# Kernel tuning notes

Hardware: AMD Instinct MI355X
Metric: run time of the kernel (lower is better)

## Reference

```python
import jax, jax.numpy as jnp
from jax import lax
import numpy as np


def setup_inputs() -> dict:
    key = jax.random.key(0)
    ks = iter(jax.random.split(key, 48))

    def w(shape):
        fan = shape[0] if len(shape) == 2 else int(np.prod(shape[1:]))
        return jax.random.normal(next(ks), shape, jnp.float32) / np.sqrt(fan)

    def b(n):
        return jax.random.normal(next(ks), (n,), jnp.float32) * 0.01

    T = 16
    return dict(
        search=jax.random.normal(next(ks), (3, 383, 287), jnp.float32),
        exemplars=jax.random.normal(next(ks), (T, 3, 383, 287), jnp.float32),
        # AlexNet features (random-weight stand-in for pretrained)
        aw1=w((64, 3, 11, 11)), ab1=b(64),
        aw2=w((192, 64, 5, 5)), ab2=b(192),
        aw3=w((384, 192, 3, 3)), ab3=b(384),
        aw4=w((256, 384, 3, 3)), ab4=b(256),
        aw5=w((256, 256, 3, 3)), ab5=b(256),
        # conv_deconv: Conv1d(256,256,3,p=1) -> MaxPool1d(88) -> ConvTranspose1d(256,256,88)
        wcd=w((256, 256, 3)), bcd=b(256),
        wt=w((256, 256, 88)), bt=b(256),
        # st_gcn: GCN(256, 512, 256)
        ws1=w((256, 512)), bs1=b(512),
        ws2=w((512, 256)), bs2=b(256),
        # g, h: 1x1 Conv1d(256,256) == linear maps
        wg=w((256, 256)), bg=b(256),
        wh=w((256, 256)), bh=b(256),
        # ct_gcn: GCN(256, 384, 256)
        wc1=w((256, 384)), bc1=b(384),
        wc2=w((384, 256)), bc2=b(256),
    )


def _gct_forward(search, exemplars, aw1, ab1, aw2, ab2, aw3, ab3, aw4, ab4,
                 aw5, ab5, wcd, bcd, wt, bt, ws1, bs1, ws2, bs2,
                 wg, bg, wh, bh, wc1, bc1, wc2, bc2):
    f32 = jnp.float32

    def conv2d(x, w, bias, s, p):
        y = lax.conv_general_dilated(x, w, (s, s), [(p, p), (p, p)],
                                     dimension_numbers=('NCHW', 'OIHW', 'NCHW'))
        return y + bias[None, :, None, None]

    def maxpool(x):  # k=3, s=2, VALID (AlexNet pools)
        return lax.reduce_window(x, -jnp.inf, lax.max, (1, 1, 3, 3), (1, 1, 2, 2), 'VALID')

    def features(x):
        x = maxpool(jax.nn.relu(conv2d(x, aw1, ab1, 4, 2)))
        x = maxpool(jax.nn.relu(conv2d(x, aw2, ab2, 1, 2)))
        x = jax.nn.relu(conv2d(x, aw3, ab3, 1, 1))
        x = jax.nn.relu(conv2d(x, aw4, ab4, 1, 1))
        x = maxpool(jax.nn.relu(conv2d(x, aw5, ab5, 1, 1)))
        return x

    lrelu = lambda v: jax.nn.leaky_relu(v, 0.01)

    X = features(search[None])          # [1,256,11,8]
    Z = features(exemplars)             # [T,256,11,8]
    T = Z.shape[0]
    D = X.shape[1]                      # 256
    M = X.shape[2] * X.shape[3]         # 88
    Xf = X.reshape(D, M)                # [256,88]
    Zf = Z.reshape(T, D, M)             # [T,256,88]

    # conv_deconv branch: conv1d(k=3,p=1) -> global maxpool -> conv_transpose(k=M)
    xc = lax.conv_general_dilated(Xf[None], wcd, (1,), [(1, 1)],
                                  dimension_numbers=('NCH', 'OIH', 'NCH'))[0] + bcd[:, None]
    v = jnp.max(xc, axis=1)                              # [256]
    X_hat = jnp.einsum('i,iok->ok', v, wt) + bt[:, None]  # [256,88]

    # spatiotemporal graph: A[i+T*j, i+T*k]=1 for j!=k; self-loops for t!=0
    TM = T * M
    n = jnp.arange(TM)
    same_t = (n[:, None] % T) == (n[None, :] % T)
    diff_s = (n[:, None] // T) != (n[None, :] // T)
    A1 = (same_t & diff_s).astype(f32) + jnp.diag((n % T != 0).astype(f32))

    # st GCN over TM nodes (node n = t + T*m -> spatial-major flatten)
    nodes = Zf.transpose(2, 0, 1).reshape(TM, D)          # [TM,256]
    h1 = lrelu(A1 @ (nodes @ ws1) + bs1)                  # [TM,512]
    h2 = lrelu(A1 @ (h1 @ ws2) + bs2)                     # [TM,256]
    V1 = jnp.max(h2.reshape(M, T, D), axis=1).T           # temporal max-pool -> [256,88]

    # dynamic cross-track graph: pairwise g/h affinities + row softmax (fused)
    Vx = V1 + X_hat                                       # [256,88]
    G = wg @ Vx + bg[:, None]                             # [256,88]
    Hh = wh @ Vx + bh[:, None]                            # [256,88]
    A2 = jax.nn.softmax(Hh.T @ G, axis=1)                 # [88,88], A2[j,i]=g(i).h(j)

    # ct GCN
    xv = V1.T                                             # [88,256]
    c1 = lrelu(A2 @ (xv @ wc1) + bc1)                     # [88,384]
    V2 = lrelu(A2 @ (c1 @ wc2) + bc2).T                   # [256,88]

    # F.conv2d(X[1,256,11,8], V2[1,256,11,8]) -> full-overlap correlation = scalar
    R = jnp.sum(Xf * V2).reshape(1, 1, 1, 1)
    return R


def reference(search, exemplars, aw1, ab1, aw2, ab2, aw3, ab3, aw4, ab4,
              aw5, ab5, wcd, bcd, wt, bt, ws1, bs1, ws2, bs2,
              wg, bg, wh, bh, wc1, bc1, wc2, bc2):
    return _gct_forward(search, exemplars, aw1, ab1, aw2, ab2, aw3, ab3, aw4, ab4,
                        aw5, ab5, wcd, bcd, wt, bt, ws1, bs1, ws2, bs2,
                        wg, bg, wh, bh, wc1, bc1, wc2, bc2)
```

## Files before the change

kernel.cpp:

```cpp
#include <hip/hip_runtime.h>
#include <hip/hip_bf16.h>
#include <math.h>

#define BATCH 17
#define T_EX 16
#define H0 383
#define W0 287
#define C1 64
#define H1 95
#define W1 71
#define H1P 47
#define W1P 35
#define C2 192
#define H2P 23
#define W2P 17
#define C3 384
#define C45 256
#define H5P 11
#define W5P 8
#define DD 256
#define MM 88
#define TM 1408

#define HP1 389
#define WP1 292

typedef unsigned short ushort_t;
typedef __attribute__((ext_vector_type(8))) short short8;
typedef __attribute__((ext_vector_type(4))) float f32x4;

__device__ __forceinline__ float lrelu(float v) { return v > 0.f ? v : 0.01f * v; }

__device__ __forceinline__ ushort_t f2bf(float f) {
    unsigned int u = __float_as_uint(f);
    unsigned int r = (u + 0x7fffu + ((u >> 16) & 1u)) >> 16;
    return (ushort_t)r;
}
__device__ __forceinline__ float b2f(ushort_t b) {
    return __uint_as_float(((unsigned int)b) << 16);
}
__device__ __forceinline__ short8 ld16(const ushort_t* p) { return *(const short8*)p; }
__device__ __forceinline__ short8 ld2x8(const ushort_t* p) {
    union { uint2 u[2]; short8 s; } uu;
    uu.u[0] = *(const uint2*)p;
    uu.u[1] = *(const uint2*)(p + 4);
    return uu.s;
}
__device__ __forceinline__ void async_cp16(ushort_t* l, const ushort_t* g) {
    __builtin_amdgcn_global_load_lds(
        (const __attribute__((address_space(1))) void*)g,
        (__attribute__((address_space(3))) void*)l, 16, 0, 0);
}

__device__ __forceinline__ void wprep_dev(const float* __restrict__ w,
                                          ushort_t* __restrict__ out,
                                          int KH, int KWl, int KWr, int CINl, int CINr,
                                          int NKS, int OCr, int idx) {
    int c = idx & 255;
    int rest = idx >> 8;
    int ks = rest % NKS;
    int ocb = rest / NKS;
    int k8 = c >> 6, m = c & 63;
    int oc = ocb * 64 + m;
    int KWC = KWl * CINl;
    ushort_t* o = out + (size_t)idx * 8;
#pragma unroll
    for (int j = 0; j < 8; ++j) {
        int kg = ks * 32 + k8 * 8 + j;
        int ky = kg / KWC; int rem = kg - ky * KWC;
        int kx = rem / CINl; int ic = rem - kx * CINl;
        float v = 0.f;
        if (oc < OCr && ky < KH && kx < KWr && ic < CINr)
            v = w[(((size_t)oc * CINr + ic) * KH + ky) * KWr + kx];
        o[j] = f2bf(v);
    }
}

__global__ void prep1_wp1_k(const float* __restrict__ search, const float* __restrict__ exemp,
                            ushort_t* __restrict__ out, const float* __restrict__ w1,
                            ushort_t* __restrict__ WT) {
    const int pb = (BATCH * HP1 * WP1 + 255) / 256;
    if ((int)blockIdx.x >= pb) {
        int idx = (blockIdx.x - pb) * 256 + threadIdx.x;
        if (idx < 4608) wprep_dev(w1, WT, 11, 12, 11, 4, 3, 18, 64, idx);
        return;
    }
    int idx = blockIdx.x * 256 + threadIdx.x;
    if (idx >= BATCH * HP1 * WP1) return;
    int x = idx % WP1; int t = idx / WP1;
    int y = t % HP1; int b = t / HP1;
    ushort4 o = {0, 0, 0, 0};
    int ix = x - 2, iy = y - 2;
    if (ix >= 0 && ix < W0 && iy >= 0 && iy < H0) {
        const float* src = (b == 0) ? search : exemp + (size_t)(b - 1) * 3 * H0 * W0;
        const int hw = H0 * W0;
        o.x = f2bf(src[iy * W0 + ix]);
        o.y = f2bf(src[hw + iy * W0 + ix]);
        o.z = f2bf(src[2 * hw + iy * W0 + ix]);
    }
    *(ushort4*)&out[(size_t)idx * 4] = o;
}

__global__ void wprep_k(const float* __restrict__ w, ushort_t* __restrict__ out,
                        int KH, int KWl, int KWr, int CINl, int CINr,
                        int NKS, int nch, int OCr,
                        float4* __restrict__ zp, int zn4) {
    const int wb = (nch + 255) >> 8;
    if ((int)blockIdx.x >= wb) {
        int z = (blockIdx.x - wb) * 256 + threadIdx.x;
        if (z < zn4) zp[z] = (float4){0.f, 0.f, 0.f, 0.f};
        return;
    }
    int idx = blockIdx.x * 256 + threadIdx.x;
    if (idx >= nch) return;
    wprep_dev(w, out, KH, KWl, KWr, CINl, CINr, NKS, OCr, idx);
}

__global__ void pool_wp_k(const ushort_t* __restrict__ in, ushort_t* __restrict__ out,
                          int C, int Hin, int Win, int Hout, int Wout,
                          int OHp, int OWp, int OPAD,
                          float4* __restrict__ zp, int zn4,
                          const float* __restrict__ w, ushort_t* __restrict__ WT,
                          int KH, int KWl, int KWr, int CINl, int CINr,
                          int NKS, int nch, int OCr) {
    const int total = BATCH * C * OHp * OWp;
    const int pb = (total + 255) >> 8;
    const int zb = (zn4 + 255) >> 8;
    int bx = blockIdx.x;
    if (bx >= pb + zb) {
        int idx = (bx - pb - zb) * 256 + threadIdx.x;
        if (idx < nch) wprep_dev(w, WT, KH, KWl, KWr, CINl, CINr, NKS, OCr, idx);
        return;
    }
    if (bx >= pb) {
        int z = (bx - pb) * 256 + threadIdx.x;
        if (z < zn4) zp[z] = (float4){0.f, 0.f, 0.f, 0.f};
        return;
    }
    int idx = bx * 256 + threadIdx.x;
    if (idx >= total) return;
    int c = idx % C; int r = idx / C;
    int x = r % OWp; r /= OWp;
    int y = r % OHp; int b = r / OHp;
    int iy = y - OPAD, ix = x - OPAD;
    ushort_t v = 0;
    if (iy >= 0 && iy < Hout && ix >= 0 && ix < Wout) {
        const int rs = Win * C;
        const ushort_t* p = in + (((size_t)b * Hin + 2 * iy) * Win + 2 * ix) * C + c;
        float m = b2f(p[0]);
        m = fmaxf(m, b2f(p[C])); m = fmaxf(m, b2f(p[2 * C]));
        m = fmaxf(m, b2f(p[rs])); m = fmaxf(m, b2f(p[rs + C])); m = fmaxf(m, b2f(p[rs + 2 * C]));
        m = fmaxf(m, b2f(p[2 * rs])); m = fmaxf(m, b2f(p[2 * rs + C])); m = fmaxf(m, b2f(p[2 * rs + 2 * C]));
        v = f2bf(m);
    }
    out[idx] = v;
}

template <int STRIDE, bool A16>
__global__ __launch_bounds__(256) void conv_mfma14(
    const ushort_t* __restrict__ inp, const ushort_t* __restrict__ wt,
    const float* __restrict__ bias, ushort_t* __restrict__ out,
    int Hp, int Wp, int C, int Wout, int HW, int Ntot, int NKS2, int KWl,
    int OHp, int OWp, int OPAD, int COUT) {
    const int tid = threadIdx.x;
    const int wv = tid >> 6, lane = tid & 63;
    const int quad = lane >> 4, l16 = lane & 15;
    const int wr = wv >> 1, wc = wv & 1;
    const int n_blk = blockIdx.x * 64;
    const int ocb = blockIdx.y;

    __shared__ ushort_t As[2][4096];
    __shared__ ushort_t Bs[2][4096];
    __shared__ int offs[432];

    const int KWC = KWl * C;
    for (int g = tid; g < NKS2 * 8; g += 256) {
        int kg = g * 8;
        int ky = kg / KWC; int rem = kg - ky * KWC;
        int kx = rem / C; int c8 = rem - kx * C;
        offs[g] = (ky * Wp + kx) * C + c8;
    }

    const size_t HWC = (size_t)Hp * Wp * C;
    const int g8 = lane & 7, po = lane >> 3;
    const ushort_t* bsrc0 = nullptr; const ushort_t* bsrc1 = nullptr;
    const ushort_t* lsrc = nullptr;
    int ws0 = 0, ws1 = 0;
    if constexpr (A16) {
        int np0 = n_blk + wv * 16 + po;      if (np0 >= Ntot) np0 = Ntot - 1;
        int np1 = n_blk + wv * 16 + 8 + po;  if (np1 >= Ntot) np1 = Ntot - 1;
        int b0 = np0 / HW, p0 = np0 - b0 * HW;
        int b1 = np1 / HW, p1 = np1 - b1 * HW;
        int oy0 = p0 / Wout, ox0 = p0 - oy0 * Wout;
        int oy1 = p1 / Wout, ox1 = p1 - oy1 * Wout;
        bsrc0 = inp + (size_t)b0 * HWC + (size_t)(oy0 * STRIDE * Wp + ox0 * STRIDE) * C;
        bsrc1 = inp + (size_t)b1 * HWC + (size_t)(oy1 * STRIDE * Wp + ox1 * STRIDE) * C;
        ws0 = g8 * 512 + (((wv * 16 + po) ^ g8) * 8);
        ws1 = g8 * 512 + (((wv * 16 + 8 + po) ^ g8) * 8);
    } else {
        int n0 = n_blk + lane; if (n0 >= Ntot) n0 = Ntot - 1;
        int b0 = n0 / HW, p0 = n0 - b0 * HW;
        int oy = p0 / Wout, ox = p0 - oy * Wout;
        lsrc = inp + (size_t)b0 * HWC + (size_t)(oy * STRIDE * Wp + ox * STRIDE) * C;
    }

    f32x4 acc[2][2];
#pragma unroll
    for (int am = 0; am < 2; ++am)
#pragma unroll
        for (int bn = 0; bn < 2; ++bn) acc[am][bn] = (f32x4){0.f, 0.f, 0.f, 0.f};

    const ushort_t* wblk = wt + (size_t)ocb * (size_t)NKS2 * 4096;

    __syncthreads();

    {
        const ushort_t* aS = wblk + tid * 8;
        async_cp16(&As[0][tid * 8], aS);
        async_cp16(&As[0][2048 + tid * 8], aS + 2048);
        if constexpr (A16) {
            *(short8*)&Bs[0][ws0] = ld16(bsrc0 + offs[g8]);
            *(short8*)&Bs[0][ws1] = ld16(bsrc1 + offs[g8]);
        } else {
            const int o0 = offs[wv], o1 = offs[4 + wv];
            *(short8*)&Bs[0][tid * 8] = ld2x8(lsrc + o0);
            *(short8*)&Bs[0][2048 + tid * 8] = ld2x8(lsrc + o1);
        }
    }
    __syncthreads();

    for (int ks2 = 0; ks2 < NKS2; ++ks2) {
        const int cur = ks2 & 1, nxt = cur ^ 1;
        const bool more = (ks2 + 1 < NKS2);
        short8 rb0, rb1;
        if (more) {
            const ushort_t* aS = wblk + (size_t)(ks2 + 1) * 4096 + tid * 8;
            async_cp16(&As[nxt][tid * 8], aS);
            async_cp16(&As[nxt][2048 + tid * 8], aS + 2048);
            if constexpr (A16) {
                rb0 = ld16(bsrc0 + offs[(ks2 + 1) * 8 + g8]);
                rb1 = ld16(bsrc1 + offs[(ks2 + 1) * 8 + g8]);
            } else {
                const int o0 = offs[(ks2 + 1) * 8 + wv], o1 = offs[(ks2 + 1) * 8 + 4 + wv];
                *(short8*)&Bs[nxt][tid * 8] = ld2x8(lsrc + o0);
                *(short8*)&Bs[nxt][2048 + tid * 8] = ld2x8(lsrc + o1);
            }
        }
#pragma unroll
        for (int h = 0; h < 2; ++h) {
            const short8 a0 = *(const short8*)&As[cur][h * 2048 + (quad * 64 + wr * 32 + l16) * 8];
            const short8 a1 = *(const short8*)&As[cur][h * 2048 + (quad * 64 + wr * 32 + 16 + l16) * 8];
            short8 b0, b1;
            if constexpr (A16) {
                b0 = *(const short8*)&Bs[cur][h * 2048 + quad * 512 + (((wc * 32 + l16) ^ (h * 4 + quad)) * 8)];
                b1 = *(const short8*)&Bs[cur][h * 2048 + quad * 512 + (((wc * 32 + 16 + l16) ^ (h * 4 + quad)) * 8)];
            } else {
                b0 = *(const short8*)&Bs[cur][h * 2048 + (quad * 64 + wc * 32 + l16) * 8];
                b1 = *(const short8*)&Bs[cur][h * 2048 + (quad * 64 + wc * 32 + 16 + l16) * 8];
            }
            acc[0][0] = __builtin_amdgcn_mfma_f32_16x16x32_bf16(a0, b0, acc[0][0], 0, 0, 0);
            acc[0][1] = __builtin_amdgcn_mfma_f32_16x16x32_bf16(a0, b1, acc[0][1], 0, 0, 0);
            acc[1][0] = __builtin_amdgcn_mfma_f32_16x16x32_bf16(a1, b0, acc[1][0], 0, 0, 0);
            acc[1][1] = __builtin_amdgcn_mfma_f32_16x16x32_bf16(a1, b1, acc[1][1], 0, 0, 0);
        }
        if constexpr (A16) {
            if (more) {
                *(short8*)&Bs[nxt][ws0] = rb0;
                *(short8*)&Bs[nxt][ws1] = rb1;
            }
        }
        __syncthreads();
    }

    const int oc0 = ocb * 64 + wr * 32 + quad * 4;
#pragma unroll
    for (int bn = 0; bn < 2; ++bn) {
        int n = n_blk + wc * 32 + bn * 16 + l16;
        if (n < Ntot) {
            int bb = n / HW; int pix = n - bb * HW;
            int y = pix / Wout, x = pix - y * Wout;
            size_t base = (((size_t)bb * OHp + y + OPAD) * OWp + x + OPAD) * COUT;
#pragma unroll
            for (int am = 0; am < 2; ++am) {
                const int oc = oc0 + am * 16;
                ushort4 o;
                o.x = f2bf(fmaxf(acc[am][bn][0] + bias[oc], 0.f));
                o.y = f2bf(fmaxf(acc[am][bn][1] + bias[oc + 1], 0.f));
                o.z = f2bf(fmaxf(acc[am][bn][2] + bias[oc + 2], 0.f));
                o.w = f2bf(fmaxf(acc[am][bn][3] + bias[oc + 3], 0.f));
                *(ushort4*)&out[base + oc] = o;
            }
        }
    }
}

template <int MODE, bool HASBIAS, bool SC1>
__device__ __forceinline__ void gemm_dev(
    ushort_t (*Bs)[2048],
    const ushort_t* __restrict__ Bsrc, const ushort_t* __restrict__ wt,
    const float* __restrict__ bias, float* __restrict__ out,
    int RS, int N, int NKS, int sn, int sc, int bx, int by) {
    const int tid = threadIdx.x;
    const int wv = tid >> 6, lane = tid & 63;
    const int quad = lane >> 4, l16 = lane & 15;
    const int n_blk = bx * 64;
    const int ocb = by;

    int n_g = n_blk + lane;
    int n_gc = n_g < N ? n_g : N - 1;
    int row = (MODE == 1) ? (1 + (n_gc & 15)) * MM + (n_gc >> 4) : n_gc;
    const size_t base0 = (size_t)row * RS;

    f32x4 acc[4];
#pragma unroll
    for (int cn = 0; cn < 4; ++cn) acc[cn] = (f32x4){0.f, 0.f, 0.f, 0.f};

    const ushort_t* wblk = wt + (size_t)ocb * NKS * 2048;
    const int afrag = (quad * 64 + wv * 16 + l16) * 8;

    short8 a0 = ld16(wblk + afrag);
    *(short8*)&Bs[0][tid * 8] = ld16(Bsrc + base0 + wv * 8);
    __syncthreads();

    for (int ks = 0; ks < NKS; ++ks) {
        const int cur = ks & 1, nxt = cur ^ 1;
        short8 a1, bn;
        const bool more = (ks + 1 < NKS);
        if (more) {
            a1 = ld16(wblk + (ks + 1) * 2048 + afrag);
            bn = ld16(Bsrc + base0 + (ks + 1) * 32 + wv * 8);
        }
#pragma unroll
        for (int cn = 0; cn < 4; ++cn) {
            const short8 bfr = *(const short8*)&Bs[cur][(quad * 64 + cn * 16 + l16) * 8];
            acc[cn] = __builtin_amdgcn_mfma_f32_16x16x32_bf16(a0, bfr, acc[cn], 0, 0, 0);
        }
        if (more) *(short8*)&Bs[nxt][tid * 8] = bn;
        a0 = a1;
        __syncthreads();
    }

    const int oc0 = ocb * 64 + wv * 16 + quad * 4;
    float bb[4] = {0.f, 0.f, 0.f, 0.f};
    if (HASBIAS) { bb[0] = bias[oc0]; bb[1] = bias[oc0+1]; bb[2] = bias[oc0+2]; bb[3] = bias[oc0+3]; }
#pragma unroll
    for (int cn = 0; cn < 4; ++cn) {
        int n = n_blk + cn * 16 + l16;
        if (n < N) {
            if (SC1) {
                float4 o;
                o.x = acc[cn][0] + bb[0]; o.y = acc[cn][1] + bb[1];
                o.z = acc[cn][2] + bb[2]; o.w = acc[cn][3] + bb[3];
                *(float4*)&out[(size_t)n * sn + oc0] = o;
            } else {
#pragma unroll
                for (int reg = 0; reg < 4; ++reg)
                    out[(size_t)n * sn + (size_t)(oc0 + reg) * sc] = acc[cn][reg] + bb[reg];
            }
        }
    }
}

template <int MODE, bool HASBIAS, bool SC1>
__global__ __launch_bounds__(256) void gemm_mfma3_k(
    const ushort_t* __restrict__ Bsrc, const ushort_t* __restrict__ wt,
    const float* __restrict__ bias, float* __restrict__ out,
    int RS, int N, int NKS, int sn, int sc) {
    __shared__ ushort_t Bs[2][2048];
    gemm_dev<MODE, HASBIAS, SC1>(Bs, Bsrc, wt, bias, out, RS, N, NKS, sn, sc,
                                 blockIdx.x, blockIdx.y);
}

__global__ __launch_bounds__(256) void gemm_pair_k(
    const ushort_t* __restrict__ XfPad, const ushort_t* __restrict__ WCDT,
    const float* __restrict__ bcd, float* __restrict__ xc,
    const ushort_t* __restrict__ PB, const ushort_t* __restrict__ WS1T,
    float* __restrict__ Y1) {
    __shared__ ushort_t Bs[2][2048];
    if (blockIdx.x < 2) {
        if (blockIdx.y < 4)
            gemm_dev<0, true, false>(Bs, XfPad, WCDT, bcd, xc, 256, MM, 24, 1, MM,
                                     blockIdx.x, blockIdx.y);
    } else {
        gemm_dev<1, false, true>(Bs, PB, WS1T, nullptr, Y1, 256, TM, 8, 512, 1,
                                 blockIdx.x - 2, blockIdx.y);
    }
}

__global__ void wg_pool5_k(const float* __restrict__ ws1, const float* __restrict__ ws2,
                           const float* __restrict__ wcd, ushort_t* __restrict__ WS1T,
                           ushort_t* __restrict__ WS2T, ushort_t* __restrict__ WCDT,
                           const ushort_t* __restrict__ in, float* __restrict__ P,
                           ushort_t* __restrict__ PB, ushort_t* __restrict__ XfPad) {
    if (blockIdx.x < 224) {
        int idx = blockIdx.x * 256 + threadIdx.x;
        const float* src; ushort_t* dst; int NKS, mode = 0, sa = 1, sk = 0, base;
        if (idx < 16384)       { src = ws1; dst = WS1T; NKS = 8;  sk = 512; base = idx; }
        else if (idx < 32768)  { src = ws2; dst = WS2T; NKS = 16; sk = 256; base = idx - 16384; }
        else                   { src = wcd; dst = WCDT; NKS = 24; mode = 1; base = idx - 32768; }
        int c = base & 255;
        int rest = base >> 8;
        int ks = rest % NKS;
        int ocb = rest / NKS;
        int k8 = c >> 6, m = c & 63;
        int oc = ocb * 64 + m;
        ushort_t* o = dst + (size_t)base * 8;
#pragma unroll
        for (int j = 0; j < 8; ++j) {
            int kg = ks * 32 + k8 * 8 + j;
            float v;
            if (mode == 0) v = src[(size_t)oc * sa + (size_t)kg * sk];
            else           v = src[(size_t)oc * 768 + (kg & 255) * 3 + (kg >> 8)];
            o[j] = f2bf(v);
        }
    } else {
        int idx = (blockIdx.x - 224) * 256 + threadIdx.x;
        if (idx >= BATCH * 256 * MM) return;
        int c = idx % 256; int r = idx / 256;
        int x = r % W5P; r /= W5P;
        int y = r % H5P; int b = r / H5P;
        const int rs = W2P * 256;
        const ushort_t* p = in + (((size_t)b * H2P + 2 * y) * W2P + 2 * x) * 256 + c;
        float m = b2f(p[0]);
        m = fmaxf(m, b2f(p[256])); m = fmaxf(m, b2f(p[512]));
        m = fmaxf(m, b2f(p[rs])); m = fmaxf(m, b2f(p[rs + 256])); m = fmaxf(m, b2f(p[rs + 512]));
        m = fmaxf(m, b2f(p[2 * rs])); m = fmaxf(m, b2f(p[2 * rs + 256])); m = fmaxf(m, b2f(p[2 * rs + 512]));
        int mm = y * W5P + x;
        size_t o = ((size_t)b * MM + mm) * 256 + c;
        P[o] = m;
        ushort_t mb = f2bf(m);
        PB[o] = mb;
        if (b == 0) XfPad[(size_t)(mm + 1) * 256 + c] = mb;
    }
}

__global__ void xhat_sh1_k(const float* __restrict__ xc, const float* __restrict__ wt,
                           const float* __restrict__ bt, float* __restrict__ xhat,
                           const float* __restrict__ Y1, const float* __restrict__ bs1,
                           ushort_t* __restrict__ h1b) {
    if (blockIdx.x < 88) {
        __shared__ float lv[256];
        {
            int j = threadIdx.x;
            const float* xr = xc + (size_t)j * MM;
            float mx = xr[0];
            for (int k = 1; k < MM; ++k) mx = fmaxf(mx, xr[k]);
            lv[j] = mx;
        }
        __syncthreads();
        int idx = blockIdx.x * 256 + threadIdx.x;
        if (idx >= DD * MM) return;
        int k = idx % MM, o = idx / MM;
        float acc = bt[o];
        for (int i = 0; i < 256; ++i) acc = fmaf(lv[i], wt[(i * 256 + o) * MM + k], acc);
        xhat[idx] = acc;
    } else {
        int idx = (blockIdx.x - 88) * 256 + threadIdx.x;
        if (idx >= T_EX * 512) return;
        int c = idx & 511, t = idx >> 9;
        float s = 0.f;
        for (int m = 0; m < MM; ++m) s += Y1[(size_t)(m * T_EX + t) * 512 + c];
        float base = s + bs1[c];
        if (t == 0) {
            for (int m = 0; m < MM; ++m) {
                float val = base - Y1[(size_t)(m * T_EX) * 512 + c];
                h1b[(size_t)(m * T_EX) * 512 + c] = f2bf(lrelu(val));
            }
        } else {
            ushort_t v = f2bf(lrelu(base));
            for (int m = 0; m < MM; ++m)
                h1b[(size_t)(m * T_EX + t) * 512 + c] = v;
        }
    }
}

__global__ void sh2v1_k(const float* __restrict__ Y2, const float* __restrict__ bs2,
                        const float* __restrict__ xhat,
                        float* __restrict__ V1, float* __restrict__ Vx) {
    int d = blockIdx.x;
    int tid = threadIdx.x;
    __shared__ float S2s[16];
    if (tid < 16) {
        float s = 0.f;
        for (int m = 0; m < MM; ++m) s += Y2[(size_t)(m * T_EX + tid) * 256 + d];
        S2s[tid] = s + bs2[d];
    }
    __syncthreads();
    for (int m = tid; m < MM; m += 128) {
        float y0 = Y2[(size_t)(m * T_EX) * 256 + d];
        float mx = -INFINITY;
        for (int t = 0; t < T_EX; ++t) {
            float val = (t == 0) ? lrelu(S2s[0] - y0) : lrelu(S2s[t]);
            mx = fmaxf(mx, val);
        }
        int idx = d * MM + m;
        V1[idx] = mx;
        Vx[idx] = mx + xhat[idx];
    }
}

__global__ void lin_t1_k(const float* __restrict__ Wgm, const float* __restrict__ bg,
                         const float* __restrict__ Whm, const float* __restrict__ bh,
                         const float* __restrict__ Vx, float* __restrict__ G,
                         float* __restrict__ Hh,
                         const float* __restrict__ V1, const float* __restrict__ wc1,
                         float* __restrict__ t1) {
    int bx = blockIdx.x;
    if (bx < 176) {
        int sel = bx >= 88;
        int idx = (bx - (sel ? 88 : 0)) * 256 + threadIdx.x;
        if (idx >= DD * MM) return;
        const float* W = sel ? Whm : Wgm;
        const float* bias = sel ? bh : bg;
        float* out = sel ? Hh : G;
        int m = idx % MM, o = idx / MM;
        const float* wr = W + o * 256;
        float acc = bias[o];
        for (int i = 0; i < 256; ++i) acc = fmaf(wr[i], Vx[i * MM + m], acc);
        out[idx] = acc;
    } else {
        int idx = (bx - 176) * 256 + threadIdx.x;
        if (idx >= MM * 384) return;
        int c = idx % 384, m = idx / 384;
        float acc = 0.f;
        for (int d = 0; d < 256; ++d) acc = fmaf(V1[d * MM + m], wc1[d * 384 + c], acc);
        t1[idx] = acc;
    }
}

__global__ void smsm_k(const float* __restrict__ Hh, const float* __restrict__ G,
                       float* __restrict__ A2) {
    int j = blockIdx.x;
    int tid = threadIdx.x;
    __shared__ float row[96];
    __shared__ float red[128];
    for (int i = tid; i < MM; i += 128) {
        float acc = 0.f;
        for (int c = 0; c < 256; ++c) acc = fmaf(Hh[c * MM + j], G[c * MM + i], acc);
        row[i] = acc;
    }
    __syncthreads();
    float val = (tid < MM) ? row[tid] : -INFINITY;
    red[tid] = val; __syncthreads();
    for (int s = 64; s > 0; s >>= 1) {
        if (tid < s) red[tid] = fmaxf(red[tid], red[tid + s]);
        __syncthreads();
    }
    float mx = red[0]; __syncthreads();
    float e = (tid < MM) ? expf(val - mx) : 0.f;
    red[tid] = e; __syncthreads();
    for (int s = 64; s > 0; s >>= 1) {
        if (tid < s) red[tid] += red[tid + s];
        __syncthreads();
    }
    float inv = 1.f / red[0];
    if (tid < MM) A2[j * MM + tid] = e * inv;
}

__global__ void c1_k(const float* __restrict__ A2, const float* __restrict__ t1,
                     const float* __restrict__ bc1, float* __restrict__ c1,
                     unsigned* __restrict__ cnt) {
    if (blockIdx.x == 0 && threadIdx.x == 0) *cnt = 0u;
    int idx = blockIdx.x * 256 + threadIdx.x;
    if (idx >= MM * 384) return;
    int c = idx % 384, j = idx / 384;
    float acc = bc1[c];
    for (int i = 0; i < MM; ++i) acc = fmaf(A2[j * MM + i], t1[i * 384 + c], acc);
    c1[idx] = lrelu(acc);
}

__global__ void t2_k(const float* __restrict__ c1, const float* __restrict__ wc2,
                     float* __restrict__ t2) {
    int idx = blockIdx.x * 256 + threadIdx.x;
    if (idx >= MM * 256) return;
    int c = idx % 256, m = idx / 256;
    const float* cr = c1 + m * 384;
    float acc = 0.f;
    for (int d = 0; d < 384; ++d) acc = fmaf(cr[d], wc2[d * 256 + c], acc);
    t2[idx] = acc;
}

__global__ __launch_bounds__(256) void v2f_k(const float* __restrict__ A2,
                                             const float* __restrict__ t2,
                                             const float* __restrict__ bc2,
                                             const float* __restrict__ Xf2,
                                             float* __restrict__ V2m,
                                             unsigned* __restrict__ cnt,
                                             float* __restrict__ out) {
    int j = blockIdx.x;
    int tid = threadIdx.x;
    __shared__ float a2row[88];
    if (tid < 88) a2row[tid] = A2[j * MM + tid];
    __syncthreads();
    {
        int c = tid;
        float acc = bc2[c];
        for (int i = 0; i < MM; ++i) acc = fmaf(a2row[i], t2[i * 256 + c], acc);
        V2m[(size_t)j * 256 + c] = lrelu(acc);
    }
    __threadfence();
    __syncthreads();
    __shared__ bool last;
    if (tid == 0) last = (atomicAdd(cnt, 1u) == 87u);
    __syncthreads();
    if (last) {
        __threadfence();
        __shared__ float red[256];
        float acc = 0.f;
        for (int idx = tid; idx < DD * MM; idx += 256)
            acc = fmaf(Xf2[idx], V2m[idx], acc);
        red[tid] = acc; __syncthreads();
        for (int s = 128; s > 0; s >>= 1) {
            if (tid < s) red[tid] += red[tid + s];
            __syncthreads();
        }
        if (tid == 0) out[0] = red[0];
    }
}

extern "C" void kernel_launch(void* const* d_in, const int* in_sizes, int n_in,
                              void* d_out, int out_size, void* d_ws, size_t ws_size,
                              hipStream_t stream) {
    const float* search = (const float*)d_in[0];
    const float* exemp  = (const float*)d_in[1];
    const float* aw1 = (const float*)d_in[2];  const float* ab1 = (const float*)d_in[3];
    const float* aw2 = (const float*)d_in[4];  const float* ab2 = (const float*)d_in[5];
    const float* aw3 = (const float*)d_in[6];  const float* ab3 = (const float*)d_in[7];
    const float* aw4 = (const float*)d_in[8];  const float* ab4 = (const float*)d_in[9];
    const float* aw5 = (const float*)d_in[10]; const float* ab5 = (const float*)d_in[11];
    const float* wcd = (const float*)d_in[12]; const float* bcd = (const float*)d_in[13];
    const float* wt  = (const float*)d_in[14]; const float* bt  = (const float*)d_in[15];
    const float* ws1 = (const float*)d_in[16]; const float* bs1 = (const float*)d_in[17];
    const float* ws2 = (const float*)d_in[18]; const float* bs2 = (const float*)d_in[19];
    const float* wg  = (const float*)d_in[20]; const float* bg  = (const float*)d_in[21];
    const float* wh  = (const float*)d_in[22]; const float* bh  = (const float*)d_in[23];
    const float* wc1 = (const float*)d_in[24]; const float* bc1 = (const float*)d_in[25];
    const float* wc2 = (const float*)d_in[26]; const float* bc2 = (const float*)d_in[27];

    float* ws = (float*)d_ws;
    float* R1 = ws;
    float* R2 = ws + 3870720;
    float* R3 = ws + 7544832;
    float* Wg = ws + 8628864;

    ushort_t* in1p  = (ushort_t*)R1;
    ushort_t* c1out = (ushort_t*)R2;
    ushort_t* p1out = (ushort_t*)R3;
    ushort_t* c2out = (ushort_t*)R1;
    ushort_t* p2out = (ushort_t*)R2;
    ushort_t* c3out = (ushort_t*)(R2 + 775200);
    ushort_t* c4out = (ushort_t*)R1;
    ushort_t* c5out = (ushort_t*)R3;
    ushort_t* WT    = (ushort_t*)Wg;

    prep1_wp1_k<<<7543 + 18, 256, 0, stream>>>(search, exemp, in1p, aw1, WT);
    conv_mfma14<4, false><<<dim3(1792, 1), 256, 0, stream>>>(
        in1p, WT, ab1, c1out, HP1, WP1, 4, W1, H1 * W1, BATCH * H1 * W1, 9, 12, H1, W1, 0, 64);
    pool_wp_k<<<8454 + 150, 256, 0, stream>>>(
        c1out, p1out, 64, H1, W1, H1P, W1P, 51, 39, 2, nullptr, 0,
        aw2, WT, 5, 5, 5, 64, 64, 50, 38400, 192);
    conv_mfma14<1, true><<<dim3(437, 3), 256, 0, stream>>>(
        p1out, WT, ab2, c2out, 51, 39, 64, W1P, H1P * W1P, BATCH * H1P * W1P, 25, 5, H1P, W1P, 0, 192);
    pool_wp_k<<<6057 + 1515 + 324, 256, 0, stream>>>(
        c2out, p2out, 192, H1P, W1P, H2P, W2P, 25, 19, 1,
        (float4*)(R2 + 775200), 387600,
        aw3, WT, 3, 3, 3, 192, 192, 54, 82944, 384);
    conv_mfma14<1, true><<<dim3(104, 6), 256, 0, stream>>>(
        p2out, WT, ab3, c3out, 25, 19, 192, W2P, H2P * W2P, BATCH * H2P * W2P, 27, 3, 25, 19, 1, 384);
    wprep_k<<<432 + 1010, 256, 0, stream>>>(aw4, WT, 3, 3, 3, 384, 384, 108, 110592, 256,
                                            (float4*)R1, 258400);
    conv_mfma14<1, true><<<dim3(104, 4), 256, 0, stream>>>(
        c3out, WT, ab4, c4out, 25, 19, 384, W2P, H2P * W2P, BATCH * H2P * W2P, 54, 3, 25, 19, 1, 256);
    wprep_k<<<288, 256, 0, stream>>>(aw5, WT, 3, 3, 3, 256, 256, 72, 73728, 256, nullptr, 0);
    conv_mfma14<1, true><<<dim3(104, 4), 256, 0, stream>>>(
        c4out, WT, ab5, c5out, 25, 19, 256, W2P, H2P * W2P, BATCH * H2P * W2P, 36, 3, H2P, W2P, 0, 256);

    float*    P      = R1 + 2417664;
    ushort_t* PB     = (ushort_t*)(R1 + 2800640);
    ushort_t* XfPad  = (ushort_t*)(R1 + 2992128);
    float*    xc     = R1 + 3003648;

    ushort_t* WS1T = (ushort_t*)Wg;
    ushort_t* WS2T = (ushort_t*)(Wg + 65536);
    ushort_t* WCDT = (ushort_t*)(Wg + 131072);

    wg_pool5_k<<<224 + (BATCH * 256 * MM + 255) / 256, 256, 0, stream>>>(
        ws1, ws2, wcd, WS1T, WS2T, WCDT, c5out, P, PB, XfPad);
    float* Xf2 = P;

    float* xhat = R1 + 1024;
    float* Y1   = R1 + 23552;
    ushort_t* h1b = (ushort_t*)(R1 + 752640);
    float* Y2   = R1 + 1473536;
    float* V1   = R1 + 2198528;
    float* Vx   = R1 + 2221056;
    float* G    = R1 + 2243584;
    float* Hh   = R1 + 2266112;
    float* A2   = R1 + 2296832;
    float* t1   = R1 + 2305024;
    float* c1   = R1 + 2338816;
    float* t2   = R1 + 2372608;
    float* V2m  = R1 + 2395136;
    unsigned* cnt = (unsigned*)(R1 + 512);

    gemm_pair_k<<<dim3(24, 8), 256, 0, stream>>>(XfPad, WCDT, bcd, xc, PB, WS1T, Y1);
    xhat_sh1_k<<<120, 256, 0, stream>>>(xc, wt, bt, xhat, Y1, bs1, h1b);

    gemm_mfma3_k<0, false, true><<<dim3(22, 4), 256, 0, stream>>>(
        h1b, WS2T, nullptr, Y2, 512, TM, 16, 256, 1);
    sh2v1_k<<<256, 128, 0, stream>>>(Y2, bs2, xhat, V1, Vx);

    lin_t1_k<<<308, 256, 0, stream>>>(wg, bg, wh, bh, Vx, G, Hh, V1, wc1, t1);
    smsm_k<<<MM, 128, 0, stream>>>(Hh, G, A2);

    c1_k<<<132, 256, 0, stream>>>(A2, t1, bc1, c1, cnt);
    t2_k<<<88, 256, 0, stream>>>(c1, wc2, t2);
    v2f_k<<<MM, 256, 0, stream>>>(A2, t2, bc2, Xf2, V2m, cnt, (float*)d_out);
}
```

Measured before the change: 457.6 us.

## Consolidate weight prep into one kernel and zero only conv pad borders

All remaining weight repacks (conv3-5, GCN and conv-deconv weights) are folded into the pool2 kernel, with each weight set given its own workspace buffer. This removes the separate wprep launches and the weight-prep half of the pool5 kernel. Full-buffer zeroing of the padded conv3/conv4 outputs is replaced by extra blocks in the preceding conv launch that zero only the one-pixel border ring. The aim is fewer launches and less memory-fill traffic, at the cost of more buffer aliasing and extra idle blocks in the conv grids.

```diff
diff --git a/kernel.cpp b/kernel.cpp
--- a/kernel.cpp
+++ b/kernel.cpp
@@ -101,40 +101,18 @@
     *(ushort4*)&out[(size_t)idx * 4] = o;
 }
 
-__global__ void wprep_k(const float* __restrict__ w, ushort_t* __restrict__ out,
-                        int KH, int KWl, int KWr, int CINl, int CINr,
-                        int NKS, int nch, int OCr,
-                        float4* __restrict__ zp, int zn4) {
-    const int wb = (nch + 255) >> 8;
-    if ((int)blockIdx.x >= wb) {
-        int z = (blockIdx.x - wb) * 256 + threadIdx.x;
-        if (z < zn4) zp[z] = (float4){0.f, 0.f, 0.f, 0.f};
-        return;
-    }
-    int idx = blockIdx.x * 256 + threadIdx.x;
-    if (idx >= nch) return;
-    wprep_dev(w, out, KH, KWl, KWr, CINl, CINr, NKS, OCr, idx);
-}
-
 __global__ void pool_wp_k(const ushort_t* __restrict__ in, ushort_t* __restrict__ out,
                           int C, int Hin, int Win, int Hout, int Wout,
                           int OHp, int OWp, int OPAD,
-                          float4* __restrict__ zp, int zn4,
                           const float* __restrict__ w, ushort_t* __restrict__ WT,
                           int KH, int KWl, int KWr, int CINl, int CINr,
                           int NKS, int nch, int OCr) {
     const int total = BATCH * C * OHp * OWp;
     const int pb = (total + 255) >> 8;
-    const int zb = (zn4 + 255) >> 8;
     int bx = blockIdx.x;
-    if (bx >= pb + zb) {
-        int idx = (bx - pb - zb) * 256 + threadIdx.x;
+    if (bx >= pb) {
+        int idx = (bx - pb) * 256 + threadIdx.x;
         if (idx < nch) wprep_dev(w, WT, KH, KWl, KWr, CINl, CINr, NKS, OCr, idx);
-        return;
-    }
-    if (bx >= pb) {
-        int z = (bx - pb) * 256 + threadIdx.x;
-        if (z < zn4) zp[z] = (float4){0.f, 0.f, 0.f, 0.f};
         return;
     }
     int idx = bx * 256 + threadIdx.x;
@@ -156,13 +134,95 @@
     out[idx] = v;
 }
 
+__global__ void pool_wp2big_k(const ushort_t* __restrict__ in, ushort_t* __restrict__ out,
+                              const float* __restrict__ aw3, ushort_t* __restrict__ WT,
+                              const float* __restrict__ aw4, ushort_t* __restrict__ WT2,
+                              const float* __restrict__ aw5, ushort_t* __restrict__ WT3,
+                              const float* __restrict__ ws1, const float* __restrict__ ws2,
+                              const float* __restrict__ wcd, ushort_t* __restrict__ WS1T,
+                              ushort_t* __restrict__ WS2T, ushort_t* __restrict__ WCDT) {
+    int bx = blockIdx.x;
+    if (bx < 6057) {
+        int idx = bx * 256 + threadIdx.x;
+        const int total = BATCH * 192 * 25 * 19;
+        if (idx >= total) return;
+        int c = idx % 192; int r = idx / 192;
+        int x = r % 19; r /= 19;
+        int y = r % 25; int b = r / 25;
+        int iy = y - 1, ix = x - 1;
+        ushort_t v = 0;
+        if (iy >= 0 && iy < H2P && ix >= 0 && ix < W2P) {
+            const int rs = W1P * 192;
+            const ushort_t* p = in + (((size_t)b * H1P + 2 * iy) * W1P + 2 * ix) * 192 + c;
+            float m = b2f(p[0]);
+            m = fmaxf(m, b2f(p[192])); m = fmaxf(m, b2f(p[384]));
+            m = fmaxf(m, b2f(p[rs])); m = fmaxf(m, b2f(p[rs + 192])); m = fmaxf(m, b2f(p[rs + 384]));
+            m = fmaxf(m, b2f(p[2 * rs])); m = fmaxf(m, b2f(p[2 * rs + 192])); m = fmaxf(m, b2f(p[2 * rs + 384]));
+            v = f2bf(m);
+        }
+        out[idx] = v;
+    } else if (bx < 6381) {
+        int idx = (bx - 6057) * 256 + threadIdx.x;
+        if (idx < 82944) wprep_dev(aw3, WT, 3, 3, 3, 192, 192, 54, 384, idx);
+    } else if (bx < 6813) {
+        int idx = (bx - 6381) * 256 + threadIdx.x;
+        if (idx < 110592) wprep_dev(aw4, WT2, 3, 3, 3, 384, 384, 108, 256, idx);
+    } else if (bx < 7101) {
+        int idx = (bx - 6813) * 256 + threadIdx.x;
+        if (idx < 73728) wprep_dev(aw5, WT3, 3, 3, 3, 256, 256, 72, 256, idx);
+    } else {
+        int idx = (bx - 7101) * 256 + threadIdx.x;
+        if (idx >= 57344) return;
+        const float* src; ushort_t* dst; int NKS, mode = 0, sk = 0, base;
+        if (idx < 16384)       { src = ws1; dst = WS1T; NKS = 8;  sk = 512; base = idx; }
+        else if (idx < 32768)  { src = ws2; dst = WS2T; NKS = 16; sk = 256; base = idx - 16384; }
+        else                   { src = wcd; dst = WCDT; NKS = 24; mode = 1; base = idx - 32768; }
+        int c = base & 255;
+        int rest = base >> 8;
+        int ks = rest % NKS;
+        int ocb = rest / NKS;
+        int k8 = c >> 6, m = c & 63;
+        int oc = ocb * 64 + m;
+        ushort_t* o = dst + (size_t)base * 8;
+#pragma unroll
+        for (int j = 0; j < 8; ++j) {
+            int kg = ks * 32 + k8 * 8 + j;
+            float v;
+            if (mode == 0) v = src[(size_t)oc + (size_t)kg * sk];
+            else           v = src[(size_t)oc * 768 + (kg & 255) * 3 + (kg >> 8)];
+            o[j] = f2bf(v);
+        }
+    }
+}
+
 template <int STRIDE, bool A16>
 __global__ __launch_bounds__(256) void conv_mfma14(
     const ushort_t* __restrict__ inp, const ushort_t* __restrict__ wt,
     const float* __restrict__ bias, ushort_t* __restrict__ out,
     int Hp, int Wp, int C, int Wout, int HW, int Ntot, int NKS2, int KWl,
-    int OHp, int OWp, int OPAD, int COUT) {
+    int OHp, int OWp, int OPAD, int COUT,
+    int NBX, ushort_t* __restrict__ ringp, int ringChunks, int ringC) {
     const int tid = threadIdx.x;
+    if ((int)blockIdx.x >= NBX) {
+        if (blockIdx.y == 0 && ringp) {
+            int idx = ((int)blockIdx.x - NBX) * 256 + tid;
+            if (idx < ringChunks) {
+                int pc = ringC >> 3;
+                int b = idx / (84 * pc);
+                int r = idx - b * 84 * pc;
+                int rp = r / pc;
+                int c8 = (r - rp * pc) * 8;
+                int y, x;
+                if (rp < 19)      { y = 0;  x = rp; }
+                else if (rp < 38) { y = 24; x = rp - 19; }
+                else if (rp < 61) { y = rp - 38 + 1; x = 0; }
+                else              { y = rp - 61 + 1; x = 18; }
+                short8 z = {0, 0, 0, 0, 0, 0, 0, 0};
+                *(short8*)&ringp[(((size_t)b * 25 + y) * 19 + x) * ringC + c8] = z;
+            }
+        }
+        return;
+    }
     const int wv = tid >> 6, lane = tid & 63;
     const int quad = lane >> 4, l16 = lane & 15;
     const int wr = wv >> 1, wc = wv & 1;
@@ -387,51 +447,25 @@
     }
 }
 
-__global__ void wg_pool5_k(const float* __restrict__ ws1, const float* __restrict__ ws2,
-                           const float* __restrict__ wcd, ushort_t* __restrict__ WS1T,
-                           ushort_t* __restrict__ WS2T, ushort_t* __restrict__ WCDT,
-                           const ushort_t* __restrict__ in, float* __restrict__ P,
-                           ushort_t* __restrict__ PB, ushort_t* __restrict__ XfPad) {
-    if (blockIdx.x < 224) {
-        int idx = blockIdx.x * 256 + threadIdx.x;
-        const float* src; ushort_t* dst; int NKS, mode = 0, sa = 1, sk = 0, base;
-        if (idx < 16384)       { src = ws1; dst = WS1T; NKS = 8;  sk = 512; base = idx; }
-        else if (idx < 32768)  { src = ws2; dst = WS2T; NKS = 16; sk = 256; base = idx - 16384; }
-        else                   { src = wcd; dst = WCDT; NKS = 24; mode = 1; base = idx - 32768; }
-        int c = base & 255;
-        int rest = base >> 8;
-        int ks = rest % NKS;
-        int ocb = rest / NKS;
-        int k8 = c >> 6, m = c & 63;
-        int oc = ocb * 64 + m;
-        ushort_t* o = dst + (size_t)base * 8;
-#pragma unroll
-        for (int j = 0; j < 8; ++j) {
-            int kg = ks * 32 + k8 * 8 + j;
-            float v;
-            if (mode == 0) v = src[(size_t)oc * sa + (size_t)kg * sk];
-            else           v = src[(size_t)oc * 768 + (kg & 255) * 3 + (kg >> 8)];
-            o[j] = f2bf(v);
-        }
-    } else {
-        int idx = (blockIdx.x - 224) * 256 + threadIdx.x;
-        if (idx >= BATCH * 256 * MM) return;
-        int c = idx % 256; int r = idx / 256;
-        int x = r % W5P; r /= W5P;
-        int y = r % H5P; int b = r / H5P;
-        const int rs = W2P * 256;
-        const ushort_t* p = in + (((size_t)b * H2P + 2 * y) * W2P + 2 * x) * 256 + c;
-        float m = b2f(p[0]);
-        m = fmaxf(m, b2f(p[256])); m = fmaxf(m, b2f(p[512]));
-        m = fmaxf(m, b2f(p[rs])); m = fmaxf(m, b2f(p[rs + 256])); m = fmaxf(m, b2f(p[rs + 512]));
-        m = fmaxf(m, b2f(p[2 * rs])); m = fmaxf(m, b2f(p[2 * rs + 256])); m = fmaxf(m, b2f(p[2 * rs + 512]));
-        int mm = y * W5P + x;
-        size_t o = ((size_t)b * MM + mm) * 256 + c;
-        P[o] = m;
-        ushort_t mb = f2bf(m);
-        PB[o] = mb;
-        if (b == 0) XfPad[(size_t)(mm + 1) * 256 + c] = mb;
-    }
+__global__ void pool5_k(const ushort_t* __restrict__ in, float* __restrict__ P,
+                        ushort_t* __restrict__ PB, ushort_t* __restrict__ XfPad) {
+    int idx = blockIdx.x * 256 + threadIdx.x;
+    if (idx >= BATCH * 256 * MM) return;
+    int c = idx % 256; int r = idx / 256;
+    int x = r % W5P; r /= W5P;
+    int y = r % H5P; int b = r / H5P;
+    const int rs = W2P * 256;
+    const ushort_t* p = in + (((size_t)b * H2P + 2 * y) * W2P + 2 * x) * 256 + c;
+    float m = b2f(p[0]);
+    m = fmaxf(m, b2f(p[256])); m = fmaxf(m, b2f(p[512]));
+    m = fmaxf(m, b2f(p[rs])); m = fmaxf(m, b2f(p[rs + 256])); m = fmaxf(m, b2f(p[rs + 512]));
+    m = fmaxf(m, b2f(p[2 * rs])); m = fmaxf(m, b2f(p[2 * rs + 256])); m = fmaxf(m, b2f(p[2 * rs + 512]));
+    int mm = y * W5P + x;
+    size_t o = ((size_t)b * MM + mm) * 256 + c;
+    P[o] = m;
+    ushort_t mb = f2bf(m);
+    PB[o] = mb;
+    if (b == 0) XfPad[(size_t)(mm + 1) * 256 + c] = mb;
 }
 
 __global__ void xhat_sh1_k(const float* __restrict__ xc, const float* __restrict__ wt,
@@ -652,40 +686,40 @@
     ushort_t* c4out = (ushort_t*)R1;
     ushort_t* c5out = (ushort_t*)R3;
     ushort_t* WT    = (ushort_t*)Wg;
+    ushort_t* WT2   = (ushort_t*)(R1 + 2800640);
+    ushort_t* WT3   = (ushort_t*)(R1 + 3243008);
+    ushort_t* WS1T  = (ushort_t*)(R1 + 3537920);
+    ushort_t* WS2T  = (ushort_t*)(R1 + 3603456);
+    ushort_t* WCDT  = (ushort_t*)(R1 + 3668992);
 
     prep1_wp1_k<<<7543 + 18, 256, 0, stream>>>(search, exemp, in1p, aw1, WT);
     conv_mfma14<4, false><<<dim3(1792, 1), 256, 0, stream>>>(
-        in1p, WT, ab1, c1out, HP1, WP1, 4, W1, H1 * W1, BATCH * H1 * W1, 9, 12, H1, W1, 0, 64);
+        in1p, WT, ab1, c1out, HP1, WP1, 4, W1, H1 * W1, BATCH * H1 * W1, 9, 12, H1, W1, 0, 64,
+        1792, nullptr, 0, 0);
     pool_wp_k<<<8454 + 150, 256, 0, stream>>>(
-        c1out, p1out, 64, H1, W1, H1P, W1P, 51, 39, 2, nullptr, 0,
+        c1out, p1out, 64, H1, W1, H1P, W1P, 51, 39, 2,
         aw2, WT, 5, 5, 5, 64, 64, 50, 38400, 192);
     conv_mfma14<1, true><<<dim3(437, 3), 256, 0, stream>>>(
-        p1out, WT, ab2, c2out, 51, 39, 64, W1P, H1P * W1P, BATCH * H1P * W1P, 25, 5, H1P, W1P, 0, 192);
-    pool_wp_k<<<6057 + 1515 + 324, 256, 0, stream>>>(
-        c2out, p2out, 192, H1P, W1P, H2P, W2P, 25, 19, 1,
-        (float4*)(R2 + 775200), 387600,
-        aw3, WT, 3, 3, 3, 192, 192, 54, 82944, 384);
-    conv_mfma14<1, true><<<dim3(104, 6), 256, 0, stream>>>(
-        p2out, WT, ab3, c3out, 25, 19, 192, W2P, H2P * W2P, BATCH * H2P * W2P, 27, 3, 25, 19, 1, 384);
-    wprep_k<<<432 + 1010, 256, 0, stream>>>(aw4, WT, 3, 3, 3, 384, 384, 108, 110592, 256,
-                                            (float4*)R1, 258400);
+        p1out, WT, ab2, c2out, 51, 39, 64, W1P, H1P * W1P, BATCH * H1P * W1P, 25, 5, H1P, W1P, 0, 192,
+        437, nullptr, 0, 0);
+    pool_wp2big_k<<<7325, 256, 0, stream>>>(
+        c2out, p2out, aw3, WT, aw4, WT2, aw5, WT3, ws1, ws2, wcd, WS1T, WS2T, WCDT);
+    conv_mfma14<1, true><<<dim3(104 + 268, 6), 256, 0, stream>>>(
+        p2out, WT, ab3, c3out, 25, 19, 192, W2P, H2P * W2P, BATCH * H2P * W2P, 27, 3, 25, 19, 1, 384,
+        104, c3out, 68544, 384);
+    conv_mfma14<1, true><<<dim3(104 + 179, 4), 256, 0, stream>>>(
+        c3out, WT2, ab4, c4out, 25, 19, 384, W2P, H2P * W2P, BATCH * H2P * W2P, 54, 3, 25, 19, 1, 256,
+        104, c4out, 45696, 256);
     conv_mfma14<1, true><<<dim3(104, 4), 256, 0, stream>>>(
-        c3out, WT, ab4, c4out, 25, 19, 384, W2P, H2P * W2P, BATCH * H2P * W2P, 54, 3, 25, 19, 1, 256);
-    wprep_k<<<288, 256, 0, stream>>>(aw5, WT, 3, 3, 3, 256, 256, 72, 73728, 256, nullptr, 0);
-    conv_mfma14<1, true><<<dim3(104, 4), 256, 0, stream>>>(
-        c4out, WT, ab5, c5out, 25, 19, 256, W2P, H2P * W2P, BATCH * H2P * W2P, 36, 3, H2P, W2P, 0, 256);
+        c4out, WT3, ab5, c5out, 25, 19, 256, W2P, H2P * W2P, BATCH * H2P * W2P, 36, 3, H2P, W2P, 0, 256,
+        104, nullptr, 0, 0);
 
     float*    P      = R1 + 2417664;
     ushort_t* PB     = (ushort_t*)(R1 + 2800640);
     ushort_t* XfPad  = (ushort_t*)(R1 + 2992128);
     float*    xc     = R1 + 3003648;
 
-    ushort_t* WS1T = (ushort_t*)Wg;
-    ushort_t* WS2T = (ushort_t*)(Wg + 65536);
-    ushort_t* WCDT = (ushort_t*)(Wg + 131072);
-
-    wg_pool5_k<<<224 + (BATCH * 256 * MM + 255) / 256, 256, 0, stream>>>(
-        ws1, ws2, wcd, WS1T, WS2T, WCDT, c5out, P, PB, XfPad);
+    pool5_k<<<1496, 256, 0, stream>>>(c5out, P, PB, XfPad);
     float* Xf2 = P;
 
     float* xhat = R1 + 1024;
```

After: 470.5 us. +2.8%, slower.
